# Kernel tuning notes

Measured on AMD Instinct MI355X. Metric: run time of the kernel, lower is better.

Reference implementation:

```python
import jax, jax.numpy as jnp
import numpy as np

B, N, L, S, H, E, D = 4, 7, 512, 512, 8, 64, 64

def setup_inputs() -> dict:
    key = jax.random.key(0)
    kq, kk, kv = jax.random.split(key, 3)
    queries = jax.random.normal(kq, (B, N, L, H, E), dtype=jnp.float32)
    keys = jax.random.normal(kk, (B, N, S, H, E), dtype=jnp.float32)
    values = jax.random.normal(kv, (B, N, S, H, D), dtype=jnp.float32)
    return {"queries": queries, "keys": keys, "values": values}

def reference(queries, keys, values):
    # queries: [B,N,L,H,E], keys: [B,N,S,H,E], values: [B,N,S,H,D]
    E_ = queries.shape[-1]
    scale = 1.0 / jnp.sqrt(jnp.asarray(E_, dtype=queries.dtype))
    # scores: [B,N,H,L,S]
    scores = jnp.einsum('bnlhe,bnshe->bnhls', queries, keys)
    attn = jax.nn.softmax(scale * scores, axis=-1)  # dropout p=0 (eval)
    V = jnp.einsum('bnhls,bnshd->bnlhd', attn, values)
    return V
```

## Files before the change

kernel.cpp:

```cpp
#include <hip/hip_runtime.h>

#define B_ 4
#define N_ 7
#define L_ 512
#define S_ 512
#define H_ 8
#define E_ 64
#define D_ 64

constexpr int QT = 128;
constexpr int ST = 128;
constexpr int KP = 72;
constexpr int VP = ST + 4;

typedef _Float16 f16x8 __attribute__((ext_vector_type(8)));
typedef _Float16 f16x4 __attribute__((ext_vector_type(4)));
typedef float    f32x4 __attribute__((ext_vector_type(4)));

__global__ __launch_bounds__(512, 4)
void attn_fwd(const float* __restrict__ Q, const float* __restrict__ K,
              const float* __restrict__ V, float* __restrict__ O)
{
    __shared__ _Float16 Ks[ST * KP];
    __shared__ _Float16 Vs[D_ * VP];

    const int bnh   = blockIdx.y;
    const int h     = bnh & (H_ - 1);
    const int bn    = bnh >> 3;
    const int qbase = blockIdx.x * QT;

    const int tid  = threadIdx.x;
    const int wid  = tid >> 6;
    const int lane = tid & 63;
    const int quad = lane >> 4;
    const int m16  = lane & 15;

    const float* Qp = Q + ((size_t)bn * L_ * H_ + h) * E_;
    const float* Kp = K + ((size_t)bn * S_ * H_ + h) * E_;
    const float* Vp = V + ((size_t)bn * S_ * H_ + h) * D_;
    float*       Op = O + ((size_t)bn * L_ * H_ + h) * E_;

    const float qsc = 0.125f * 1.4426950408889634f;
    f16x8 qf[2];
    #pragma unroll
    for (int kt = 0; kt < 2; ++kt) {
        const float* p = Qp + (size_t)(qbase + wid*16 + m16) * (H_*E_) + kt*32 + quad*8;
        float4 a = *(const float4*)p;
        float4 b = *(const float4*)(p + 4);
        f16x8 f;
        f[0]=(_Float16)(a.x*qsc); f[1]=(_Float16)(a.y*qsc);
        f[2]=(_Float16)(a.z*qsc); f[3]=(_Float16)(a.w*qsc);
        f[4]=(_Float16)(b.x*qsc); f[5]=(_Float16)(b.y*qsc);
        f[6]=(_Float16)(b.z*qsc); f[7]=(_Float16)(b.w*qsc);
        qf[kt] = f;
    }

    const f32x4 fzero = {0.f, 0.f, 0.f, 0.f};
    f32x4 of[4];
    #pragma unroll
    for (int dt = 0; dt < 4; ++dt) of[dt] = fzero;

    float m_run = -1e30f;
    float l_run = 0.f;

    for (int sb = 0; sb < S_; sb += ST) {
        __syncthreads();

        #pragma unroll
        for (int j = 0; j < 4; ++j) {
            int idx = j*512 + tid;
            int r = idx >> 4, c = (idx & 15) * 4;
            float4 v = *(const float4*)(Kp + (size_t)(sb + r)*(H_*E_) + c);
            f16x4 w;
            w[0]=(_Float16)v.x; w[1]=(_Float16)v.y; w[2]=(_Float16)v.z; w[3]=(_Float16)v.w;
            *(f16x4*)&Ks[r*KP + c] = w;
        }
        #pragma unroll
        for (int j = 0; j < 4; ++j) {
            int idx = j*512 + tid;
            int r = idx >> 4, d = (idx & 15) * 4;
            float4 v = *(const float4*)(Vp + (size_t)(sb + r)*(H_*D_) + d);
            Vs[(d+0)*VP + r] = (_Float16)v.x;
            Vs[(d+1)*VP + r] = (_Float16)v.y;
            Vs[(d+2)*VP + r] = (_Float16)v.z;
            Vs[(d+3)*VP + r] = (_Float16)v.w;
        }
        __syncthreads();

        f32x4 acc[8];
        #pragma unroll
        for (int st = 0; st < 8; ++st) acc[st] = fzero;
        #pragma unroll
        for (int st = 0; st < 8; ++st) {
            #pragma unroll
            for (int kt = 0; kt < 2; ++kt) {
                f16x8 kf = *(const f16x8*)&Ks[(st*16 + m16)*KP + kt*32 + quad*8];
                acc[st] = __builtin_amdgcn_mfma_f32_16x16x32_f16(kf, qf[kt], acc[st], 0,0,0);
            }
        }

        {
            float mt = -1e30f;
            #pragma unroll
            for (int st = 0; st < 8; ++st)
                mt = fmaxf(mt, fmaxf(fmaxf(acc[st][0], acc[st][1]),
                                     fmaxf(acc[st][2], acc[st][3])));
            mt = fmaxf(mt, __shfl_xor(mt, 16));
            mt = fmaxf(mt, __shfl_xor(mt, 32));
            float mnew  = fmaxf(m_run, mt);
            float alpha = exp2f(m_run - mnew);
            float rsum = 0.f;
            #pragma unroll
            for (int st = 0; st < 8; ++st)
                #pragma unroll
                for (int r = 0; r < 4; ++r) {
                    float p = exp2f(acc[st][r] - mnew);
                    acc[st][r] = p;
                    rsum += p;
                }
            rsum += __shfl_xor(rsum, 16);
            rsum += __shfl_xor(rsum, 32);
            l_run = l_run * alpha + rsum;
            m_run = mnew;
            #pragma unroll
            for (int r = 0; r < 4; ++r) {
                float aO = __shfl(alpha, quad*4 + r);
                #pragma unroll
                for (int dt = 0; dt < 4; ++dt) of[dt][r] *= aO;
            }
        }

        #pragma unroll
        for (int st = 0; st < 8; ++st) {
            f16x4 pf;
            pf[0]=(_Float16)acc[st][0]; pf[1]=(_Float16)acc[st][1];
            pf[2]=(_Float16)acc[st][2]; pf[3]=(_Float16)acc[st][3];
            #pragma unroll
            for (int dt = 0; dt < 4; ++dt) {
                f16x4 vf = *(const f16x4*)&Vs[(dt*16 + m16)*VP + st*16 + quad*4];
                of[dt] = __builtin_amdgcn_mfma_f32_16x16x16f16(pf, vf, of[dt], 0,0,0);
            }
        }
    }

    #pragma unroll
    for (int r = 0; r < 4; ++r) {
        float inv = 1.0f / __shfl(l_run, quad*4 + r);
        float* op = Op + (size_t)(qbase + wid*16 + quad*4 + r)*(H_*D_) + m16;
        #pragma unroll
        for (int dt = 0; dt < 4; ++dt)
            op[dt*16] = of[dt][r] * inv;
    }
}

extern "C" void kernel_launch(void* const* d_in, const int* in_sizes, int n_in,
                              void* d_out, int out_size, void* d_ws, size_t ws_size,
                              hipStream_t stream)
{
    const float* Q = (const float*)d_in[0];
    const float* K = (const float*)d_in[1];
    const float* V = (const float*)d_in[2];
    float* O = (float*)d_out;
    dim3 grid(L_ / QT, B_ * N_ * H_);
    attn_fwd<<<grid, 512, 0, stream>>>(Q, K, V, O);
}
```

Baseline: 159.6 us.

## Double-buffer K/V tiles with register prefetch, swizzle V LDS, reorder grid

The K/V shared-memory tiles are now double-buffered. The next tile's global loads are issued into registers before the current tile's MFMA work and stored to the alternate buffer afterwards, so each iteration needs one barrier instead of two and global latency can overlap compute. The transposed V layout gets an XOR swizzle on the row index to reduce LDS bank conflicts on the scattered stores, and the grid axes are swapped so blocks sharing a head are spread differently. The costs are double the LDS footprint, which may lower occupancy, and extra registers held for the prefetched tile.

```diff
diff --git a/kernel.cpp b/kernel.cpp
--- a/kernel.cpp
+++ b/kernel.cpp
@@ -10,8 +10,9 @@
 
 constexpr int QT = 128;
 constexpr int ST = 128;
+constexpr int NT = S_ / ST;
 constexpr int KP = 72;
-constexpr int VP = ST + 4;
+constexpr int VP = 132;
 
 typedef _Float16 f16x8 __attribute__((ext_vector_type(8)));
 typedef _Float16 f16x4 __attribute__((ext_vector_type(4)));
@@ -21,13 +22,13 @@
 void attn_fwd(const float* __restrict__ Q, const float* __restrict__ K,
               const float* __restrict__ V, float* __restrict__ O)
 {
-    __shared__ _Float16 Ks[ST * KP];
-    __shared__ _Float16 Vs[D_ * VP];
+    __shared__ _Float16 Ks[2][ST * KP];
+    __shared__ _Float16 Vs[2][D_ * VP];
 
-    const int bnh   = blockIdx.y;
+    const int bnh   = blockIdx.x;
     const int h     = bnh & (H_ - 1);
     const int bn    = bnh >> 3;
-    const int qbase = blockIdx.x * QT;
+    const int qbase = blockIdx.y * QT;
 
     const int tid  = threadIdx.x;
     const int wid  = tid >> 6;
@@ -38,7 +39,35 @@
     const float* Qp = Q + ((size_t)bn * L_ * H_ + h) * E_;
     const float* Kp = K + ((size_t)bn * S_ * H_ + h) * E_;
     const float* Vp = V + ((size_t)bn * S_ * H_ + h) * D_;
-    float*       Op = O + ((size_t)bn * L_ * H_ + h) * E_;
+    float*       Op = O + ((size_t)bn * L_ * H_ + h) * D_;
+
+    const int sr = tid >> 4;
+    const int sc = (tid & 15) * 4;
+    const int vswz = sc & 28;
+
+    auto load_tile = [&](int sb, float4 (&kreg)[4], float4 (&vreg)[4]) {
+        #pragma unroll
+        for (int j = 0; j < 4; ++j) {
+            int r = j * 32 + sr;
+            kreg[j] = *(const float4*)(Kp + (size_t)(sb + r) * (H_*E_) + sc);
+            vreg[j] = *(const float4*)(Vp + (size_t)(sb + r) * (H_*D_) + sc);
+        }
+    };
+    auto store_tile = [&](int buf, const float4 (&kreg)[4], const float4 (&vreg)[4]) {
+        #pragma unroll
+        for (int j = 0; j < 4; ++j) {
+            int r = j * 32 + sr;
+            f16x4 w;
+            w[0]=(_Float16)kreg[j].x; w[1]=(_Float16)kreg[j].y;
+            w[2]=(_Float16)kreg[j].z; w[3]=(_Float16)kreg[j].w;
+            *(f16x4*)&Ks[buf][r*KP + sc] = w;
+            int rs = r ^ vswz;
+            Vs[buf][(sc+0)*VP + rs] = (_Float16)vreg[j].x;
+            Vs[buf][(sc+1)*VP + rs] = (_Float16)vreg[j].y;
+            Vs[buf][(sc+2)*VP + rs] = (_Float16)vreg[j].z;
+            Vs[buf][(sc+3)*VP + rs] = (_Float16)vreg[j].w;
+        }
+    };
 
     const float qsc = 0.125f * 1.4426950408889634f;
     f16x8 qf[2];
@@ -63,29 +92,16 @@
     float m_run = -1e30f;
     float l_run = 0.f;
 
-    for (int sb = 0; sb < S_; sb += ST) {
-        __syncthreads();
+    float4 kreg[4], vreg[4];
+    load_tile(0, kreg, vreg);
+    store_tile(0, kreg, vreg);
+    __syncthreads();
 
-        #pragma unroll
-        for (int j = 0; j < 4; ++j) {
-            int idx = j*512 + tid;
-            int r = idx >> 4, c = (idx & 15) * 4;
-            float4 v = *(const float4*)(Kp + (size_t)(sb + r)*(H_*E_) + c);
-            f16x4 w;
-            w[0]=(_Float16)v.x; w[1]=(_Float16)v.y; w[2]=(_Float16)v.z; w[3]=(_Float16)v.w;
-            *(f16x4*)&Ks[r*KP + c] = w;
-        }
-        #pragma unroll
-        for (int j = 0; j < 4; ++j) {
-            int idx = j*512 + tid;
-            int r = idx >> 4, d = (idx & 15) * 4;
-            float4 v = *(const float4*)(Vp + (size_t)(sb + r)*(H_*D_) + d);
-            Vs[(d+0)*VP + r] = (_Float16)v.x;
-            Vs[(d+1)*VP + r] = (_Float16)v.y;
-            Vs[(d+2)*VP + r] = (_Float16)v.z;
-            Vs[(d+3)*VP + r] = (_Float16)v.w;
-        }
-        __syncthreads();
+    #pragma unroll
+    for (int it = 0; it < NT; ++it) {
+        const int cur = it & 1;
+
+        if (it + 1 < NT) load_tile((it + 1) * ST, kreg, vreg);
 
         f32x4 acc[8];
         #pragma unroll
@@ -94,7 +110,7 @@
         for (int st = 0; st < 8; ++st) {
             #pragma unroll
             for (int kt = 0; kt < 2; ++kt) {
-                f16x8 kf = *(const f16x8*)&Ks[(st*16 + m16)*KP + kt*32 + quad*8];
+                f16x8 kf = *(const f16x8*)&Ks[cur][(st*16 + m16)*KP + kt*32 + quad*8];
                 acc[st] = __builtin_amdgcn_mfma_f32_16x16x32_f16(kf, qf[kt], acc[st], 0,0,0);
             }
         }
@@ -137,9 +153,15 @@
             pf[2]=(_Float16)acc[st][2]; pf[3]=(_Float16)acc[st][3];
             #pragma unroll
             for (int dt = 0; dt < 4; ++dt) {
-                f16x4 vf = *(const f16x4*)&Vs[(dt*16 + m16)*VP + st*16 + quad*4];
+                int d  = dt*16 + m16;
+                f16x4 vf = *(const f16x4*)&Vs[cur][d*VP + ((st*16 + quad*4) ^ (d & 28))];
                 of[dt] = __builtin_amdgcn_mfma_f32_16x16x16f16(pf, vf, of[dt], 0,0,0);
             }
+        }
+
+        if (it + 1 < NT) {
+            store_tile(cur ^ 1, kreg, vreg);
+            __syncthreads();
         }
     }
 
@@ -161,6 +183,6 @@
     const float* K = (const float*)d_in[1];
     const float* V = (const float*)d_in[2];
     float* O = (float*)d_out;
-    dim3 grid(L_ / QT, B_ * N_ * H_);
+    dim3 grid(B_ * N_ * H_, L_ / QT);
     attn_fwd<<<grid, 512, 0, stream>>>(Q, K, V, O);
 }
```

Result: slower. 186.3 us (+16.7%).
